# Kernel optimization log

Hardware: AMD Instinct MI355X
Metric: run time of the kernel (lower is better)

Reference implementation:

```python
import jax, jax.numpy as jnp
import numpy as np

B, S, E, H = 8, 1024, 1024, 16  # batch, seq, embed, heads; head_dim = E//H = 64

def setup_inputs() -> dict:
    key = jax.random.key(0)
    k1, k2, k3 = jax.random.split(key, 3)
    x = jax.random.normal(k1, (B, S, E), dtype=jnp.float32)
    W_attn = jax.random.normal(k2, (E, 3 * E), dtype=jnp.float32) * (1.0 / np.sqrt(E))
    W_proj = jax.random.normal(k3, (E, E), dtype=jnp.float32) * (1.0 / np.sqrt(E))
    return {"x": x, "W_attn": W_attn, "W_proj": W_proj}

def reference(x, W_attn, W_proj):
    b, s, e = x.shape
    d = e // H
    qkv = x @ W_attn                      # [b, s, 3e]
    q, k, v = jnp.split(qkv, 3, axis=-1)
    q = q.reshape(b, s, H, d)
    k = k.reshape(b, s, H, d)
    v = v.reshape(b, s, H, d)
    scale = 1.0 / np.sqrt(d).astype(np.float32)
    scores = jnp.einsum('bqhd,bkhd->bhqk', q, k) * scale  # [b, H, s, s]
    causal = jnp.tril(jnp.ones((s, s), dtype=bool))
    scores = jnp.where(causal[None, None, :, :], scores, -jnp.inf)
    attn = jax.nn.softmax(scores, axis=-1)
    y = jnp.einsum('bhqk,bkhd->bqhd', attn, v).reshape(b, s, e)
    return y @ W_proj
```

## Files before the change

### kernel.cpp

```cpp
#include <hip/hip_runtime.h>
#include <hip/hip_bf16.h>

typedef unsigned short u16;
typedef __attribute__((ext_vector_type(8))) short short8;
typedef __attribute__((ext_vector_type(4))) float f32x4;
typedef __attribute__((ext_vector_type(16))) float f32x16;
typedef __attribute__((ext_vector_type(4))) unsigned short u16x4;

#define DEVINL __device__ __forceinline__

DEVINL u16 f2bf(float f) {
    union { float f; unsigned u; } x; x.f = f;
    unsigned u = x.u;
    u += 0x7fffu + ((u >> 16) & 1u);
    return (u16)(u >> 16);
}

DEVINL void gload_lds16(const void* g, void* l) {
    __builtin_amdgcn_global_load_lds(
        (const __attribute__((address_space(1))) unsigned*)g,
        (__attribute__((address_space(3))) unsigned*)l, 16, 0, 0);
}

DEVINL int swz(int row) { return (((row & 7) ^ ((row >> 3) & 7)) << 4); }

DEVINL void swap32(unsigned& a, unsigned& b) {
#if __has_builtin(__builtin_amdgcn_permlane32_swap)
    typedef __attribute__((ext_vector_type(2))) unsigned uv2;
    uv2 r = __builtin_amdgcn_permlane32_swap(a, b, false, false);
    a = r.x; b = r.y;
#else
    int h = ((int)(threadIdx.x & 63)) >> 5;
    unsigned pa = (unsigned)__shfl_xor((int)a, 32);
    unsigned pb = (unsigned)__shfl_xor((int)b, 32);
    unsigned na = h ? pb : a;
    unsigned nb = h ? b : pa;
    a = na; b = nb;
#endif
}

__global__ __launch_bounds__(256)
void k_prep(const float* __restrict__ x, const float* __restrict__ Wa,
            const float* __restrict__ Wp,
            u16* __restrict__ xb, u16* __restrict__ waT, u16* __restrict__ wpT) {
    __shared__ float t[32][33];
    const int blk = blockIdx.x;
    const int tid = threadIdx.x;
    if (blk < 2048) {
        int i = blk * 256 + tid;
        const int stride = 2048 * 256;
        #pragma unroll
        for (int it = 0; it < 4; it++, i += stride) {
            float4 v = ((const float4*)x)[i];
            u16x4 o;
            o.x = f2bf(v.x); o.y = f2bf(v.y); o.z = f2bf(v.z); o.w = f2bf(v.w);
            ((u16x4*)xb)[i] = o;
        }
    } else if (blk < 5120) {
        const int b  = blk - 2048;
        const int bx = b % 96, by = b / 96;
        const int c0 = bx * 32, r0 = by * 32;
        const int tx = tid & 31, ty = tid >> 5;
        #pragma unroll
        for (int j = 0; j < 32; j += 8)
            t[ty + j][tx] = Wa[(size_t)(r0 + ty + j) * 3072 + c0 + tx];
        __syncthreads();
        #pragma unroll
        for (int j = 0; j < 32; j += 8)
            waT[(size_t)(c0 + ty + j) * 1024 + r0 + tx] = f2bf(t[tx][ty + j]);
    } else {
        const int b  = blk - 5120;
        const int bx = b & 31, by = b >> 5;
        const int c0 = bx * 32, r0 = by * 32;
        const int tx = tid & 31, ty = tid >> 5;
        #pragma unroll
        for (int j = 0; j < 32; j += 8)
            t[ty + j][tx] = Wp[(size_t)(r0 + ty + j) * 1024 + c0 + tx];
        __syncthreads();
        #pragma unroll
        for (int j = 0; j < 32; j += 8)
            wpT[(size_t)(c0 + ty + j) * 1024 + r0 + tx] = f2bf(t[tx][ty + j]);
    }
}

__global__ void k_transpose_bf(const float* __restrict__ in, u16* __restrict__ out, int R, int C) {
    __shared__ float t[32][33];
    int c0 = blockIdx.x * 32, r0 = blockIdx.y * 32;
    int tx = threadIdx.x, ty = threadIdx.y;
    #pragma unroll
    for (int j = 0; j < 32; j += 8)
        t[ty + j][tx] = in[(size_t)(r0 + ty + j) * C + c0 + tx];
    __syncthreads();
    #pragma unroll
    for (int j = 0; j < 32; j += 8)
        out[(size_t)(c0 + ty + j) * R + r0 + tx] = f2bf(t[tx][ty + j]);
}

__global__ __launch_bounds__(256, 2)
void k_gemmT(const u16* __restrict__ A, const u16* __restrict__ BT,
             u16* __restrict__ C, int N, int K) {
    __shared__ char lds[2 * 40960];

    const int tid  = threadIdx.x;
    const int lane = tid & 63;
    const int lo   = lane & 15;
    const int hi   = lane >> 4;
    const int wave = tid >> 6;
    const int wm   = wave >> 1;
    const int wn   = wave & 1;

    const int gx   = gridDim.x;
    const int nwg  = gx * gridDim.y;
    const int orig = blockIdx.y * gx + blockIdx.x;
    const int wg   = (orig & 7) * (nwg >> 3) + (orig >> 3);
    const long row0 = (long)(wg / gx) * 128;
    const long col0 = (long)(wg % gx) * 192;

    const int NT = K >> 6;

    const int srow = tid >> 3;
    const int gsb  = ((tid & 7) ^ (srow & 7)) << 4;

    auto stage = [&](int t) {
        char* base = lds + (t & 1) * 40960;
        #pragma unroll
        for (int c = 0; c < 4; c++)
            gload_lds16((const char*)(A + (row0 + c * 32 + srow) * (size_t)K + t * 64) + gsb,
                        base + c * 4096 + tid * 16);
        #pragma unroll
        for (int c = 0; c < 6; c++)
            gload_lds16((const char*)(BT + (col0 + c * 32 + srow) * (size_t)K + t * 64) + gsb,
                        base + 16384 + c * 4096 + tid * 16);
    };

    f32x4 acc[4][6] = {};

    stage(0);
    asm volatile("s_waitcnt vmcnt(0)" ::: "memory");
    __builtin_amdgcn_s_barrier();

    for (int t = 0; t < NT; t++) {
        if (t + 1 < NT) stage(t + 1);
        const char* ab = lds + (t & 1) * 40960;
        const char* bb = ab + 16384;
        short8 af[2][4], bf[2][6];
        #pragma unroll
        for (int kk = 0; kk < 2; kk++) {
            #pragma unroll
            for (int m = 0; m < 4; m++) {
                int r = wm * 64 + m * 16 + lo;
                af[kk][m] = *(const short8*)(ab + r * 128 + ((kk * 64 + hi * 16) ^ ((r & 7) << 4)));
            }
            #pragma unroll
            for (int n = 0; n < 6; n++) {
                int r = wn * 96 + n * 16 + lo;
                bf[kk][n] = *(const short8*)(bb + r * 128 + ((kk * 64 + hi * 16) ^ ((r & 7) << 4)));
            }
        }
        #pragma unroll
        for (int m = 0; m < 4; m++)
            #pragma unroll
            for (int n = 0; n < 6; n++)
                acc[m][n] = __builtin_amdgcn_mfma_f32_16x16x32_bf16(af[0][m], bf[0][n], acc[m][n], 0, 0, 0);
        if (t + 1 < NT) {
            asm volatile("s_waitcnt vmcnt(0)" ::: "memory");
            __builtin_amdgcn_s_barrier();
        }
        #pragma unroll
        for (int m = 0; m < 4; m++)
            #pragma unroll
            for (int n = 0; n < 6; n++)
                acc[m][n] = __builtin_amdgcn_mfma_f32_16x16x32_bf16(af[1][m], bf[1][n], acc[m][n], 0, 0, 0);
    }

    #pragma unroll
    for (int m = 0; m < 4; m++)
        #pragma unroll
        for (int n = 0; n < 6; n++)
            #pragma unroll
            for (int r = 0; r < 4; r++) {
                long row = row0 + wm * 64 + m * 16 + hi * 4 + r;
                long col = col0 + wn * 96 + n * 16 + lo;
                C[row * (size_t)N + col] = f2bf(acc[m][n][r]);
            }
}

template<bool OUT_BF16>
__global__ __launch_bounds__(256, 2)
void k_gemm2(const u16* __restrict__ A, const u16* __restrict__ BT,
             void* __restrict__ C, int N, int K) {
    __shared__ char lds[2 * 32768];

    const int tid  = threadIdx.x;
    const int lane = tid & 63;
    const int lo   = lane & 15;
    const int hi   = lane >> 4;
    const int wave = tid >> 6;
    const int wm   = wave >> 1;
    const int wn   = wave & 1;

    const int gx   = gridDim.x;
    const int nwg  = gx * gridDim.y;
    const int orig = blockIdx.y * gx + blockIdx.x;
    const int wg   = (orig & 7) * (nwg >> 3) + (orig >> 3);
    const long row0 = (long)(wg / gx) * 128;
    const long col0 = (long)(wg % gx) * 128;

    const int NT = K >> 6;

    const int srow = tid >> 3;
    const int gsb  = ((tid & 7) ^ (srow & 7)) << 4;

    auto stage = [&](int t) {
        char* base = lds + (t & 1) * 32768;
        #pragma unroll
        for (int c = 0; c < 4; c++)
            gload_lds16((const char*)(A + (row0 + c * 32 + srow) * (size_t)K + t * 64) + gsb,
                        base + c * 4096 + tid * 16);
        #pragma unroll
        for (int c = 0; c < 4; c++)
            gload_lds16((const char*)(BT + (col0 + c * 32 + srow) * (size_t)K + t * 64) + gsb,
                        base + 16384 + c * 4096 + tid * 16);
    };

    f32x4 acc[4][4] = {};

    stage(0);
    asm volatile("s_waitcnt vmcnt(0)" ::: "memory");
    __builtin_amdgcn_s_barrier();

    for (int t = 0; t < NT; t++) {
        if (t + 1 < NT) stage(t + 1);
        const char* ab = lds + (t & 1) * 32768;
        const char* bb = ab + 16384;
        short8 af[2][4], bf[2][4];
        #pragma unroll
        for (int kk = 0; kk < 2; kk++) {
            #pragma unroll
            for (int m = 0; m < 4; m++) {
                int r = wm * 64 + m * 16 + lo;
                af[kk][m] = *(const short8*)(ab + r * 128 + ((kk * 64 + hi * 16) ^ ((r & 7) << 4)));
            }
            #pragma unroll
            for (int n = 0; n < 4; n++) {
                int r = wn * 64 + n * 16 + lo;
                bf[kk][n] = *(const short8*)(bb + r * 128 + ((kk * 64 + hi * 16) ^ ((r & 7) << 4)));
            }
        }
        #pragma unroll
        for (int m = 0; m < 4; m++)
            #pragma unroll
            for (int n = 0; n < 4; n++)
                acc[m][n] = __builtin_amdgcn_mfma_f32_16x16x32_bf16(af[0][m], bf[0][n], acc[m][n], 0, 0, 0);
        if (t + 1 < NT) {
            asm volatile("s_waitcnt vmcnt(0)" ::: "memory");
            __builtin_amdgcn_s_barrier();
        }
        #pragma unroll
        for (int m = 0; m < 4; m++)
            #pragma unroll
            for (int n = 0; n < 4; n++)
                acc[m][n] = __builtin_amdgcn_mfma_f32_16x16x32_bf16(af[1][m], bf[1][n], acc[m][n], 0, 0, 0);
    }

    #pragma unroll
    for (int m = 0; m < 4; m++)
        #pragma unroll
        for (int n = 0; n < 4; n++)
            #pragma unroll
            for (int r = 0; r < 4; r++) {
                long row = row0 + wm * 64 + m * 16 + hi * 4 + r;
                long col = col0 + wn * 64 + n * 16 + lo;
                if constexpr (OUT_BF16)
                    ((u16*)C)[row * (size_t)N + col] = f2bf(acc[m][n][r]);
                else
                    ((float*)C)[row * (size_t)N + col] = acc[m][n][r];
            }
}

#define SCALE_L2E 0.18033688011112042f

__global__ __launch_bounds__(256, 2)
void k_attn(const u16* __restrict__ qkv, u16* __restrict__ y) {
    constexpr int S = 1024, E = 1024, TE = 3072;
    __shared__ char alds[2 * 16384];

    const int tid  = threadIdx.x;
    const int lane = tid & 63;
    const int l31  = lane & 31;
    const int hA   = lane >> 5;
    const int wave = tid >> 6;

    const int qi = 7 - (int)(blockIdx.x >> 7);
    const int bh = blockIdx.x & 127;
    const int b  = bh >> 4;
    const int h  = bh & 15;
    const int q0 = qi * 128;
    const size_t rowbase = (size_t)b * S;
    const int qg = q0 + wave * 32 + l31;

    short8 qf[4];
    {
        const u16* qp = qkv + (rowbase + qg) * TE + h * 64 + hA * 8;
        #pragma unroll
        for (int kd = 0; kd < 4; kd++) qf[kd] = *(const short8*)(qp + kd * 16);
    }

    f32x16 o0 = {}, o1 = {};
    float ms = -1e30f, lsum = 0.f;

    const int kr0 = (wave << 3) + (lane >> 3);
    const int kcb = (lane & 7) * 16;
    const int vkv = (tid >> 3) * 2;
    const int vdc = (tid & 7) * 8;

    auto stage = [&](int t) {
        char* base = alds + (t & 1) * 16384;
        const int kv0 = t * 64;
        #pragma unroll
        for (int it = 0; it < 2; it++) {
            int r = kr0 + it * 32;
            const char* src = (const char*)qkv
                + (((rowbase + kv0 + r) * TE + E + h * 64) << 1) + (kcb ^ swz(r));
            gload_lds16(src, base + wave * 1024 + it * 4096);
        }
        const u16* vsrc = qkv + (rowbase + kv0 + vkv) * TE + 2 * E + h * 64 + vdc;
        short8 v0 = *(const short8*)vsrc;
        short8 v1 = *(const short8*)(vsrc + TE);
        #pragma unroll
        for (int j = 0; j < 8; j++) {
            int d = vdc + j;
            unsigned val = (unsigned)(u16)v0[j] | ((unsigned)(u16)v1[j] << 16);
            *(unsigned*)(base + 8192 + d * 128 + ((vkv * 2) ^ swz(d))) = val;
        }
    };

    const int ntiles = 2 * qi + 2;
    stage(0);
    for (int t = 0; t < ntiles; ++t) {
        __syncthreads();
        if (t + 1 < ntiles) stage(t + 1);

        const char* Kt = alds + (t & 1) * 16384;
        const char* Vt = Kt + 8192;
        const int kv0 = t * 64;

        const bool active = (kv0 <= q0 + wave * 32 + 31);
        if (!active) continue;

        f32x16 s0 = {}, s1 = {};
        #pragma unroll
        for (int kd = 0; kd < 4; kd++) {
            int r0 = l31, r1 = 32 + l31;
            short8 ka0 = *(const short8*)(Kt + r0 * 128 + ((kd * 32 + hA * 16) ^ swz(r0)));
            short8 ka1 = *(const short8*)(Kt + r1 * 128 + ((kd * 32 + hA * 16) ^ swz(r1)));
            s0 = __builtin_amdgcn_mfma_f32_32x32x16_bf16(ka0, qf[kd], s0, 0, 0, 0);
            s1 = __builtin_amdgcn_mfma_f32_32x32x16_bf16(ka1, qf[kd], s1, 0, 0, 0);
        }

        if (kv0 + 63 > q0 + wave * 32) {
            #pragma unroll
            for (int r = 0; r < 16; r++) {
                int kvr = kv0 + ((r & 3) + 8 * (r >> 2) + 4 * hA);
                if (kvr > qg)      s0[r] = -1e30f;
                if (kvr + 32 > qg) s1[r] = -1e30f;
            }
        }

        float pm = s0[0];
        #pragma unroll
        for (int r = 1; r < 16; r++) pm = fmaxf(pm, s0[r]);
        #pragma unroll
        for (int r = 0; r < 16; r++) pm = fmaxf(pm, s1[r]);
        pm = fmaxf(pm, __shfl_xor(pm, 32));
        float pms = pm * SCALE_L2E;
        if (__any(pms - ms > 8.0f)) {
            float msn = fmaxf(ms, pms);
            float alpha = exp2f(ms - msn);
            ms = msn;
            lsum *= alpha;
            #pragma unroll
            for (int r = 0; r < 16; r++) { o0[r] *= alpha; o1[r] *= alpha; }
        }

        float part = 0.f;
        #pragma unroll
        for (int r = 0; r < 16; r++) {
            float p0 = exp2f(s0[r] * SCALE_L2E - ms);
            float p1 = exp2f(s1[r] * SCALE_L2E - ms);
            s0[r] = p0; s1[r] = p1;
            part += p0 + p1;
        }
        lsum += part + __shfl_xor(part, 32);

        unsigned w0[8], w1[8];
        #pragma unroll
        for (int j = 0; j < 8; j++) {
            asm("v_cvt_pk_bf16_f32 %0, %1, %2" : "=v"(w0[j]) : "v"(s0[2 * j]), "v"(s0[2 * j + 1]));
            asm("v_cvt_pk_bf16_f32 %0, %1, %2" : "=v"(w1[j]) : "v"(s1[2 * j]), "v"(s1[2 * j + 1]));
        }

        #define PV_TILE(W, ST)                                                              \
        {                                                                                   \
            _Pragma("unroll")                                                               \
            for (int kkl = 0; kkl < 2; kkl++) {                                             \
                unsigned a  = W[4 * kkl],     bsw = W[4 * kkl + 2];                         \
                unsigned a2 = W[4 * kkl + 1], b2  = W[4 * kkl + 3];                         \
                swap32(a, bsw); swap32(a2, b2);                                             \
                union { int4 i; short8 s; } u;                                              \
                u.i = make_int4((int)a, (int)a2, (int)bsw, (int)b2);                        \
                {                                                                           \
                    int row = l31;                                                          \
                    short8 va = *(const short8*)(Vt + row * 128                             \
                                  + (((ST) * 64 + kkl * 32 + hA * 16) ^ swz(row)));         \
                    o0 = __builtin_amdgcn_mfma_f32_32x32x16_bf16(va, u.s, o0, 0, 0, 0);     \
                }                                                                           \
                {                                                                           \
                    int row = 32 + l31;                                                     \
                    short8 va = *(const short8*)(Vt + row * 128                             \
                                  + (((ST) * 64 + kkl * 32 + hA * 16) ^ swz(row)));         \
                    o1 = __builtin_amdgcn_mfma_f32_32x32x16_bf16(va, u.s, o1, 0, 0, 0);     \
                }                                                                           \
            }                                                                               \
        }
        PV_TILE(w0, 0)
        PV_TILE(w1, 1)
        #undef PV_TILE
    }

    __syncthreads();
    float rinv = 1.0f / lsum;
    char* Ot = alds + wave * 4096;
    const int X = (l31 & 7) << 4;
    #pragma unroll
    for (int rq = 0; rq < 4; rq++) {
        u16x4 pk0, pk1;
        #pragma unroll
        for (int j = 0; j < 4; j++) {
            pk0[j] = f2bf(o0[4 * rq + j] * rinv);
            pk1[j] = f2bf(o1[4 * rq + j] * rinv);
        }
        *(u16x4*)(Ot + l31 * 128 + ((16 * rq + 8 * hA) ^ X))      = pk0;
        *(u16x4*)(Ot + l31 * 128 + ((64 + 16 * rq + 8 * hA) ^ X)) = pk1;
    }
    __syncthreads();
    #pragma unroll
    for (int p = 0; p < 4; p++) {
        int row = p * 8 + (lane >> 3);
        int cc  = lane & 7;
        short8 vv = *(const short8*)(Ot + row * 128 + ((cc * 16) ^ ((row & 7) << 4)));
        *(short8*)(y + (rowbase + q0 + wave * 32 + row) * E + h * 64 + cc * 8) = vv;
    }
}

extern "C" void kernel_launch(void* const* d_in, const int* in_sizes, int n_in,
                              void* d_out, int out_size, void* d_ws, size_t ws_size,
                              hipStream_t stream) {
    const float* x     = (const float*)d_in[0];
    const float* Wattn = (const float*)d_in[1];
    const float* Wproj = (const float*)d_in[2];
    float* out = (float*)d_out;

    char* ws = (char*)d_ws;
    u16* buf0 = (u16*)ws;
    u16* wT   = (u16*)(ws + 16777216);
    u16* qkv  = (u16*)(ws + 16777216 + 6291456);
    const size_t wpT_off = 16777216ull + 6291456 + 50331648;
    const bool fused_wp = ws_size >= wpT_off + 2097152;
    u16* wpT  = fused_wp ? (u16*)(ws + wpT_off) : wT;

    k_prep<<<fused_wp ? 6144 : 5120, 256, 0, stream>>>(x, Wattn, Wproj, buf0, wT, wpT);
    k_gemmT<<<dim3(3072 / 192, 8192 / 128), 256, 0, stream>>>(buf0, wT, qkv, 3072, 1024);
    if (!fused_wp) {
        k_transpose_bf<<<dim3(1024 / 32, 1024 / 32), dim3(32, 8), 0, stream>>>(Wproj, wT, 1024, 1024);
    }
    k_attn<<<dim3(1024), 256, 0, stream>>>(qkv, buf0);
    k_gemm2<false><<<dim3(1024 / 128, 8192 / 128), 256, 0, stream>>>(buf0, wpT, out, 1024, 1024);
}
```

Baseline: 125.7 us.

## Defer V tile LDS transpose-write until after compute to overlap global loads

Splits V staging into a global-load issue at the top of the iteration and an LDS transpose-write after the QK/softmax/PV compute. The next tile's V load latency is then hidden behind current-tile math rather than stalling right after issue. It also raises wave priority around the MFMA blocks with s_setprio. In exchange it keeps the prefetched V registers live across the compute, raising register pressure, and adds an explicit vmcnt(0) wait.

```diff
diff --git a/kernel.cpp b/kernel.cpp
--- a/kernel.cpp
+++ b/kernel.cpp
@@ -314,7 +314,7 @@
     const int vkv = (tid >> 3) * 2;
     const int vdc = (tid & 7) * 8;
 
-    auto stage = [&](int t) {
+    auto issue = [&](int t, short8& v0, short8& v1) {
         char* base = alds + (t & 1) * 16384;
         const int kv0 = t * 64;
         #pragma unroll
@@ -325,8 +325,11 @@
             gload_lds16(src, base + wave * 1024 + it * 4096);
         }
         const u16* vsrc = qkv + (rowbase + kv0 + vkv) * TE + 2 * E + h * 64 + vdc;
-        short8 v0 = *(const short8*)vsrc;
-        short8 v1 = *(const short8*)(vsrc + TE);
+        v0 = *(const short8*)vsrc;
+        v1 = *(const short8*)(vsrc + TE);
+    };
+    auto writeV = [&](int t, short8 v0, short8 v1) {
+        char* base = alds + (t & 1) * 16384;
         #pragma unroll
         for (int j = 0; j < 8; j++) {
             int d = vdc + j;
@@ -336,96 +339,112 @@
     };
 
     const int ntiles = 2 * qi + 2;
-    stage(0);
+    {
+        short8 v0, v1;
+        issue(0, v0, v1);
+        asm volatile("s_waitcnt vmcnt(0)" ::: "memory");
+        writeV(0, v0, v1);
+    }
     for (int t = 0; t < ntiles; ++t) {
         __syncthreads();
-        if (t + 1 < ntiles) stage(t + 1);
+        short8 nv0, nv1;
+        const bool more = (t + 1 < ntiles);
+        if (more) issue(t + 1, nv0, nv1);
 
         const char* Kt = alds + (t & 1) * 16384;
         const char* Vt = Kt + 8192;
         const int kv0 = t * 64;
 
         const bool active = (kv0 <= q0 + wave * 32 + 31);
-        if (!active) continue;
-
-        f32x16 s0 = {}, s1 = {};
-        #pragma unroll
-        for (int kd = 0; kd < 4; kd++) {
-            int r0 = l31, r1 = 32 + l31;
-            short8 ka0 = *(const short8*)(Kt + r0 * 128 + ((kd * 32 + hA * 16) ^ swz(r0)));
-            short8 ka1 = *(const short8*)(Kt + r1 * 128 + ((kd * 32 + hA * 16) ^ swz(r1)));
-            s0 = __builtin_amdgcn_mfma_f32_32x32x16_bf16(ka0, qf[kd], s0, 0, 0, 0);
-            s1 = __builtin_amdgcn_mfma_f32_32x32x16_bf16(ka1, qf[kd], s1, 0, 0, 0);
-        }
-
-        if (kv0 + 63 > q0 + wave * 32) {
+        if (active) {
+            f32x16 s0 = {}, s1 = {};
+            __builtin_amdgcn_s_setprio(1);
+            #pragma unroll
+            for (int kd = 0; kd < 4; kd++) {
+                int r0 = l31, r1 = 32 + l31;
+                short8 ka0 = *(const short8*)(Kt + r0 * 128 + ((kd * 32 + hA * 16) ^ swz(r0)));
+                short8 ka1 = *(const short8*)(Kt + r1 * 128 + ((kd * 32 + hA * 16) ^ swz(r1)));
+                s0 = __builtin_amdgcn_mfma_f32_32x32x16_bf16(ka0, qf[kd], s0, 0, 0, 0);
+                s1 = __builtin_amdgcn_mfma_f32_32x32x16_bf16(ka1, qf[kd], s1, 0, 0, 0);
+            }
+            __builtin_amdgcn_s_setprio(0);
+
+            if (kv0 + 63 > q0 + wave * 32) {
+                #pragma unroll
+                for (int r = 0; r < 16; r++) {
+                    int kvr = kv0 + ((r & 3) + 8 * (r >> 2) + 4 * hA);
+                    if (kvr > qg)      s0[r] = -1e30f;
+                    if (kvr + 32 > qg) s1[r] = -1e30f;
+                }
+            }
+
+            float pm = s0[0];
+            #pragma unroll
+            for (int r = 1; r < 16; r++) pm = fmaxf(pm, s0[r]);
+            #pragma unroll
+            for (int r = 0; r < 16; r++) pm = fmaxf(pm, s1[r]);
+            pm = fmaxf(pm, __shfl_xor(pm, 32));
+            float pms = pm * SCALE_L2E;
+            if (__any(pms - ms > 8.0f)) {
+                float msn = fmaxf(ms, pms);
+                float alpha = exp2f(ms - msn);
+                ms = msn;
+                lsum *= alpha;
+                #pragma unroll
+                for (int r = 0; r < 16; r++) { o0[r] *= alpha; o1[r] *= alpha; }
+            }
+
+            float part = 0.f;
             #pragma unroll
             for (int r = 0; r < 16; r++) {
-                int kvr = kv0 + ((r & 3) + 8 * (r >> 2) + 4 * hA);
-                if (kvr > qg)      s0[r] = -1e30f;
-                if (kvr + 32 > qg) s1[r] = -1e30f;
-            }
-        }
-
-        float pm = s0[0];
-        #pragma unroll
-        for (int r = 1; r < 16; r++) pm = fmaxf(pm, s0[r]);
-        #pragma unroll
-        for (int r = 0; r < 16; r++) pm = fmaxf(pm, s1[r]);
-        pm = fmaxf(pm, __shfl_xor(pm, 32));
-        float pms = pm * SCALE_L2E;
-        if (__any(pms - ms > 8.0f)) {
-            float msn = fmaxf(ms, pms);
-            float alpha = exp2f(ms - msn);
-            ms = msn;
-            lsum *= alpha;
-            #pragma unroll
-            for (int r = 0; r < 16; r++) { o0[r] *= alpha; o1[r] *= alpha; }
-        }
-
-        float part = 0.f;
-        #pragma unroll
-        for (int r = 0; r < 16; r++) {
-            float p0 = exp2f(s0[r] * SCALE_L2E - ms);
-            float p1 = exp2f(s1[r] * SCALE_L2E - ms);
-            s0[r] = p0; s1[r] = p1;
-            part += p0 + p1;
-        }
-        lsum += part + __shfl_xor(part, 32);
-
-        unsigned w0[8], w1[8];
-        #pragma unroll
-        for (int j = 0; j < 8; j++) {
-            asm("v_cvt_pk_bf16_f32 %0, %1, %2" : "=v"(w0[j]) : "v"(s0[2 * j]), "v"(s0[2 * j + 1]));
-            asm("v_cvt_pk_bf16_f32 %0, %1, %2" : "=v"(w1[j]) : "v"(s1[2 * j]), "v"(s1[2 * j + 1]));
-        }
-
-        #define PV_TILE(W, ST)                                                              \
-        {                                                                                   \
-            _Pragma("unroll")                                                               \
-            for (int kkl = 0; kkl < 2; kkl++) {                                             \
-                unsigned a  = W[4 * kkl],     bsw = W[4 * kkl + 2];                         \
-                unsigned a2 = W[4 * kkl + 1], b2  = W[4 * kkl + 3];                         \
-                swap32(a, bsw); swap32(a2, b2);                                             \
-                union { int4 i; short8 s; } u;                                              \
-                u.i = make_int4((int)a, (int)a2, (int)bsw, (int)b2);                        \
-                {                                                                           \
-                    int row = l31;                                                          \
-                    short8 va = *(const short8*)(Vt + row * 128                             \
-                                  + (((ST) * 64 + kkl * 32 + hA * 16) ^ swz(row)));         \
-                    o0 = __builtin_amdgcn_mfma_f32_32x32x16_bf16(va, u.s, o0, 0, 0, 0);     \
-                }                                                                           \
-                {                                                                           \
-                    int row = 32 + l31;                                                     \
-                    short8 va = *(const short8*)(Vt + row * 128                             \
-                                  + (((ST) * 64 + kkl * 32 + hA * 16) ^ swz(row)));         \
-                    o1 = __builtin_amdgcn_mfma_f32_32x32x16_bf16(va, u.s, o1, 0, 0, 0);     \
-                }                                                                           \
-            }                                                                               \
-        }
-        PV_TILE(w0, 0)
-        PV_TILE(w1, 1)
-        #undef PV_TILE
+                float p0 = exp2f(s0[r] * SCALE_L2E - ms);
+                float p1 = exp2f(s1[r] * SCALE_L2E - ms);
+                s0[r] = p0; s1[r] = p1;
+                part += p0 + p1;
+            }
+            lsum += part + __shfl_xor(part, 32);
+
+            unsigned w0[8], w1[8];
+            #pragma unroll
+            for (int j = 0; j < 8; j++) {
+                asm("v_cvt_pk_bf16_f32 %0, %1, %2" : "=v"(w0[j]) : "v"(s0[2 * j]), "v"(s0[2 * j + 1]));
+                asm("v_cvt_pk_bf16_f32 %0, %1, %2" : "=v"(w1[j]) : "v"(s1[2 * j]), "v"(s1[2 * j + 1]));
+            }
+
+            __builtin_amdgcn_s_setprio(1);
+            #define PV_TILE(W, ST)                                                              \
+            {                                                                                   \
+                _Pragma("unroll")                                                               \
+                for (int kkl = 0; kkl < 2; kkl++) {                                             \
+                    unsigned a  = W[4 * kkl],     bsw = W[4 * kkl + 2];                         \
+                    unsigned a2 = W[4 * kkl + 1], b2  = W[4 * kkl + 3];                         \
+                    swap32(a, bsw); swap32(a2, b2);                                             \
+                    union { int4 i; short8 s; } u;                                              \
+                    u.i = make_int4((int)a, (int)a2, (int)bsw, (int)b2);                        \
+                    {                                                                           \
+                        int row = l31;                                                          \
+                        short8 va = *(const short8*)(Vt + row * 128                             \
+                                      + (((ST) * 64 + kkl * 32 + hA * 16) ^ swz(row)));         \
+                        o0 = __builtin_amdgcn_mfma_f32_32x32x16_bf16(va, u.s, o0, 0, 0, 0);     \
+                    }                                                                           \
+                    {                                                                           \
+                        int row = 32 + l31;                                                     \
+                        short8 va = *(const short8*)(Vt + row * 128                             \
+                                      + (((ST) * 64 + kkl * 32 + hA * 16) ^ swz(row)));         \
+                        o1 = __builtin_amdgcn_mfma_f32_32x32x16_bf16(va, u.s, o1, 0, 0, 0);     \
+                    }                                                                           \
+                }                                                                               \
+            }
+            PV_TILE(w0, 0)
+            PV_TILE(w1, 1)
+            #undef PV_TILE
+            __builtin_amdgcn_s_setprio(0);
+        }
+
+        if (more) {
+            asm volatile("s_waitcnt vmcnt(0)" ::: "memory");
+            writeV(t + 1, nv0, nv1);
+        }
     }
 
     __syncthreads();
```

Measured after the change: 124.1 us, median of 2. Within noise of the previous version (-1.2%).
